# Performance work log

Measured on AMD Instinct MI355X. Metric: run time of the kernel, lower is better.

The kernel has to match this reference:

```python
import jax, jax.numpy as jnp
import numpy as np

M, T, D, H = 2, 2048, 1024, 16
HD = D // H
SCALE = 1.0 / np.sqrt(D).astype(np.float32)  # original divides by sqrt(emb_dim)


def setup_inputs() -> dict:
    key = jax.random.key(0)
    ks = jax.random.split(key, 8)
    def lin(k):
        kw, kb = jax.random.split(k)
        W = jax.random.normal(kw, (D, D), dtype=jnp.float32) * (1.0 / np.sqrt(D))
        b = jax.random.normal(kb, (D,), dtype=jnp.float32) * 0.01
        return W, b
    Wq, bq = lin(ks[0]); Wk, bk = lin(ks[1]); Wv, bv = lin(ks[2]); Wo, bo = lin(ks[3])
    Q = jax.random.normal(ks[4], (M, T, D), dtype=jnp.float32)
    K = jax.random.normal(ks[5], (M, T, D), dtype=jnp.float32)
    V = jax.random.normal(ks[6], (M, T, D), dtype=jnp.float32)
    mask = jnp.ones((M, 1, 1, T), dtype=jnp.int32)
    return {"Q": Q, "K": K, "V": V, "mask": mask,
            "Wq": Wq, "bq": bq, "Wk": Wk, "bk": bk,
            "Wv": Wv, "bv": bv, "Wo": Wo, "bo": bo}


def reference(Q, K, V, mask, Wq, bq, Wk, bk, Wv, bv, Wo, bo):
    m = Q.shape[0]
    # torch nn.Linear: y = x @ W.T + b
    q = (Q @ Wq.T + bq).reshape(m, -1, H, HD)  # (m, Tq, h, hd)
    k = (K @ Wk.T + bk).reshape(m, -1, H, HD)
    v = (V @ Wv.T + bv).reshape(m, -1, H, HD)
    energy = jnp.einsum('mqhd,mkhd->mhqk', q, k) * SCALE
    if mask is not None:
        energy = jnp.where(mask == 0, jnp.float32(-1e20), energy)
    attn = jax.nn.softmax(energy, axis=3)  # dropout is identity at inference
    out = jnp.einsum('mhqk,mkhd->mqhd', attn, v)  # (m, Tq, h, hd)
    concat = out.reshape(m, -1, H * HD)
    return concat @ Wo.T + bo
```

## Files before the change

kernel.cpp:

```cpp
#include <hip/hip_runtime.h>
#include <cstdint>
#include <cstddef>

#define T_SEQ 2048
#define D_EMB 1024
#define H_HEADS 16
#define MROWS 4096
#define SC2 (0.03125f * 1.44269504f)
#define MASKNEG (-1e30f)

typedef __attribute__((ext_vector_type(8))) short bf16x8;
typedef __attribute__((ext_vector_type(4))) float f32x4;
typedef __attribute__((ext_vector_type(16))) float f32x16;
typedef __attribute__((ext_vector_type(4))) unsigned short us4;

__device__ __forceinline__ unsigned short f2bf(float f) {
  union { float f; uint32_t u; } v; v.f = f;
  uint32_t u = v.u;
  return (unsigned short)((u + 0x7FFFu + ((u >> 16) & 1u)) >> 16);
}

__device__ __forceinline__ uint32_t cvtpk(float lo, float hi) {
  uint32_t r;
  asm("v_cvt_pk_bf16_f32 %0, %1, %2" : "=v"(r) : "v"(lo), "v"(hi));
  return r;
}

__device__ __forceinline__ float fexp2(float x) {
  float r;
  asm("v_exp_f32 %0, %1" : "=v"(r) : "v"(x));
  return r;
}

__device__ __forceinline__ void gl16(const void* g, void* l) {
  __builtin_amdgcn_global_load_lds(
      (const __attribute__((address_space(1))) unsigned int*)g,
      (__attribute__((address_space(3))) unsigned int*)l, 16, 0, 0);
}

__global__ __launch_bounds__(256) void cvt_all(
    const float* __restrict__ Q, const float* __restrict__ K, const float* __restrict__ V,
    const float* __restrict__ Wq, const float* __restrict__ Wk,
    const float* __restrict__ Wv, const float* __restrict__ Wo,
    unsigned short* __restrict__ Qb, unsigned short* __restrict__ Kb,
    unsigned short* __restrict__ Vb,
    unsigned short* __restrict__ Wqb, unsigned short* __restrict__ Wkb,
    unsigned short* __restrict__ Wvb, unsigned short* __restrict__ Wob) {
  int i = blockIdx.x * 256 + threadIdx.x;
  const float* src;
  unsigned short* dst;
  int j;
  if (i < 3145728) {
    int s = i >> 20;
    j = i & 1048575;
    src = (s == 0) ? Q : (s == 1) ? K : V;
    dst = (s == 0) ? Qb : (s == 1) ? Kb : Vb;
  } else {
    int k = i - 3145728;
    int s = k >> 18;
    j = k & 262143;
    src = (s == 0) ? Wq : (s == 1) ? Wk : (s == 2) ? Wv : Wo;
    dst = (s == 0) ? Wqb : (s == 1) ? Wkb : (s == 2) ? Wvb : Wob;
  }
  float4 f = ((const float4*)src)[j];
  us4 o;
  o[0] = f2bf(f.x); o[1] = f2bf(f.y); o[2] = f2bf(f.z); o[3] = f2bf(f.w);
  ((us4*)dst)[j] = o;
}

__global__ __launch_bounds__(256) void qkv_gemm(
    const unsigned short* __restrict__ Qb, const unsigned short* __restrict__ Kb,
    const unsigned short* __restrict__ Vb,
    const unsigned short* __restrict__ Wqb, const unsigned short* __restrict__ Wkb,
    const unsigned short* __restrict__ Wvb,
    const float* __restrict__ bq, const float* __restrict__ bk, const float* __restrict__ bv,
    unsigned short* __restrict__ qo, unsigned short* __restrict__ ko,
    unsigned short* __restrict__ vto) {
  const int swz = (blockIdx.x & 7) * 96 + (blockIdx.x >> 3);
  const int bx = swz & 7, by = (swz >> 3) & 31, z = swz >> 8;
  const unsigned short* A = (z == 0) ? Qb : (z == 1) ? Kb : Vb;
  const unsigned short* W = (z == 0) ? Wqb : (z == 1) ? Wkb : Wvb;
  const float* bias = (z == 0) ? bq : (z == 1) ? bk : bv;

  __shared__ __align__(16) unsigned short Asm[2][128 * 32];
  __shared__ __align__(16) unsigned short Bsm[2][128 * 32];

  const int tid = threadIdx.x;
  const int lane = tid & 63, w = tid >> 6;
  const int fq = lane >> 4, fr = lane & 15;
  const int brow = by * 128, bcol = bx * 128;
  const int wr = (w >> 1) * 64, wc = (w & 1) * 64;

  f32x4 acc[4][4] = {};

#define QKV_STAGE(buf, k0)                                                     \
  {                                                                            \
    _Pragma("unroll") for (int it = 0; it < 2; ++it) {                         \
      int idx = it * 256 + tid;                                                \
      int row = idx >> 2, ce = (idx & 3) * 8;                                  \
      gl16(&A[(size_t)(brow + row) * D_EMB + (k0) + ce],                       \
           (char*)Asm[buf] + idx * 16);                                        \
      gl16(&W[(size_t)(bcol + row) * D_EMB + (k0) + ce],                       \
           (char*)Bsm[buf] + idx * 16);                                        \
    }                                                                          \
  }

#define QKV_COMPUTE(buf)                                                       \
  {                                                                            \
    bf16x8 af[4], bfr[4];                                                      \
    _Pragma("unroll") for (int i = 0; i < 4; ++i)                              \
        af[i] = *(const bf16x8*)((const char*)Asm[buf] +                       \
                                 (wr + i * 16 + fr) * 64 + fq * 16);           \
    _Pragma("unroll") for (int j = 0; j < 4; ++j)                              \
        bfr[j] = *(const bf16x8*)((const char*)Bsm[buf] +                      \
                                  (wc + j * 16 + fr) * 64 + fq * 16);          \
    _Pragma("unroll") for (int i = 0; i < 4; ++i)                              \
        _Pragma("unroll") for (int j = 0; j < 4; ++j)                          \
            acc[i][j] = __builtin_amdgcn_mfma_f32_16x16x32_bf16(               \
                af[i], bfr[j], acc[i][j], 0, 0, 0);                            \
  }

  QKV_STAGE(0, 0);
  __syncthreads();
#pragma unroll 1
  for (int t = 0; t < 32; t += 2) {
    QKV_STAGE(1, (t + 1) * 32);
    QKV_COMPUTE(0);
    __syncthreads();
    if (t + 2 < 32) QKV_STAGE(0, (t + 2) * 32);
    QKV_COMPUTE(1);
    __syncthreads();
  }

#pragma unroll
  for (int i = 0; i < 4; ++i) {
#pragma unroll
    for (int j = 0; j < 4; ++j) {
      int r0 = brow + wr + i * 16 + fq * 4;
      int cc = bcol + wc + j * 16 + fr;
      float bb = bias[cc];
      if (z < 2) {
        unsigned short* O = (z == 0) ? qo : ko;
        float sc = (z == 0) ? SC2 : 1.0f;
#pragma unroll
        for (int q = 0; q < 4; ++q)
          O[(size_t)(r0 + q) * D_EMB + cc] = f2bf((acc[i][j][q] + bb) * sc);
      } else {
        int hh = cc >> 6, dd = cc & 63;
        int mm = r0 >> 11, tt = r0 & 2047;
        us4 pk;
#pragma unroll
        for (int q = 0; q < 4; ++q) pk[q] = f2bf(acc[i][j][q] + bb);
        *(us4*)&vto[((size_t)((mm * H_HEADS + hh) * 64 + dd)) * T_SEQ + tt] = pk;
      }
    }
  }
}

__global__ __launch_bounds__(256) void out_gemm(const unsigned short* __restrict__ Ab,
                                                const unsigned short* __restrict__ Wb,
                                                const float* __restrict__ bias,
                                                float* __restrict__ Out) {
  const int swz = (blockIdx.x & 7) * 64 + (blockIdx.x >> 3);
  const int bx = swz & 15, by = swz >> 4;

  __shared__ __align__(16) unsigned short Asm[2][128 * 32];
  __shared__ __align__(16) unsigned short Bsm[2][64 * 32];
  const int tid = threadIdx.x;
  const int lane = tid & 63, w = tid >> 6;
  const int fq = lane >> 4, fr = lane & 15;
  const int brow = by * 128, bcol = bx * 64;
  const int wr = w * 32;

  f32x4 acc[2][4] = {};

#define OUT_STAGE(buf, k0)                                                     \
  {                                                                            \
    _Pragma("unroll") for (int it = 0; it < 2; ++it) {                         \
      int idx = it * 256 + tid;                                                \
      int row = idx >> 2, ce = (idx & 3) * 8;                                  \
      gl16(&Ab[(size_t)(brow + row) * D_EMB + (k0) + ce],                      \
           (char*)Asm[buf] + idx * 16);                                        \
    }                                                                          \
    {                                                                          \
      int row = tid >> 2, ce = (tid & 3) * 8;                                  \
      gl16(&Wb[(size_t)(bcol + row) * D_EMB + (k0) + ce],                      \
           (char*)Bsm[buf] + tid * 16);                                        \
    }                                                                          \
  }

#define OUT_COMPUTE(buf)                                                       \
  {                                                                            \
    bf16x8 af[2], bfr[4];                                                      \
    _Pragma("unroll") for (int i = 0; i < 2; ++i)                              \
        af[i] = *(const bf16x8*)((const char*)Asm[buf] +                       \
                                 (wr + i * 16 + fr) * 64 + fq * 16);           \
    _Pragma("unroll") for (int j = 0; j < 4; ++j)                              \
        bfr[j] = *(const bf16x8*)((const char*)Bsm[buf] +                      \
                                  (j * 16 + fr) * 64 + fq * 16);               \
    _Pragma("unroll") for (int i = 0; i < 2; ++i)                              \
        _Pragma("unroll") for (int j = 0; j < 4; ++j)                          \
            acc[i][j] = __builtin_amdgcn_mfma_f32_16x16x32_bf16(               \
                af[i], bfr[j], acc[i][j], 0, 0, 0);                            \
  }

  OUT_STAGE(0, 0);
  __syncthreads();
#pragma unroll 1
  for (int t = 0; t < 32; t += 2) {
    OUT_STAGE(1, (t + 1) * 32);
    OUT_COMPUTE(0);
    __syncthreads();
    if (t + 2 < 32) OUT_STAGE(0, (t + 2) * 32);
    OUT_COMPUTE(1);
    __syncthreads();
  }

#pragma unroll
  for (int i = 0; i < 2; ++i)
#pragma unroll
    for (int j = 0; j < 4; ++j) {
      int r0 = brow + wr + i * 16 + fq * 4;
      int cc = bcol + j * 16 + fr;
      float bb = bias[cc];
#pragma unroll
      for (int q = 0; q < 4; ++q)
        Out[(size_t)(r0 + q) * D_EMB + cc] = acc[i][j][q] + bb;
    }
}

__global__ __launch_bounds__(256) void attn_fwd(const unsigned short* __restrict__ qb,
                                                const unsigned short* __restrict__ kb,
                                                const unsigned short* __restrict__ vtb,
                                                const int* __restrict__ maskg,
                                                unsigned short* __restrict__ outb) {
  const int swzb = (blockIdx.x & 7) * 64 + (blockIdx.x >> 3);
  const int qt = swzb & 15, h = (swzb >> 4) & 15, mI = swzb >> 8;
  const int tid = threadIdx.x;
  const int lane = tid & 63, w = tid >> 6;
  const int lq = lane & 31, h2 = lane >> 5;
  const int xk = (lq & 7) << 4;
  const int vx = (lq & 7) << 4;

  __shared__ __align__(16) unsigned short Ksm[128 * 64];
  __shared__ __align__(16) unsigned short Vsm[64 * 128];
  __shared__ __align__(16) char Pw[4][2304];
  __shared__ __align__(16) float Msm[128];
  __shared__ int moks[16];

  char* KsmB = (char*)Ksm;
  char* VsmB = (char*)Vsm;
  char* PwB = Pw[w];

  if (tid < 16) moks[tid] = 1;
  __syncthreads();
  {
    int bad = 0;
    const int4* mg = (const int4*)&maskg[mI * T_SEQ + tid * 8];
    int4 a = mg[0], b = mg[1];
    bad |= (a.x == 0) | (a.y == 0) | (a.z == 0) | (a.w == 0);
    bad |= (b.x == 0) | (b.y == 0) | (b.z == 0) | (b.w == 0);
    if (bad) moks[tid >> 4] = 0;
  }
  __syncthreads();
  int okbits = 0;
#pragma unroll
  for (int i = 0; i < 16; ++i) okbits |= (moks[i] != 0) << i;

  const int qrow = qt * 128 + w * 32 + lq;
  bf16x8 qf[4];
#pragma unroll
  for (int db = 0; db < 4; ++db)
    qf[db] = *(const bf16x8*)&qb[((size_t)(mI * T_SEQ) + qrow) * D_EMB + h * 64 + db * 16 + h2 * 8];

  f32x16 oacc[2] = {};
  f32x16 liv = {};

  const unsigned short* kpan = kb + (size_t)(mI * T_SEQ) * D_EMB + h * 64;
  const unsigned short* vpan = vtb + (size_t)(mI * H_HEADS + h) * 64 * T_SEQ;

#pragma unroll 1
  for (int k0 = 0; k0 < T_SEQ; k0 += 128) {
    const int ok = (okbits >> (k0 >> 7)) & 1;
#pragma unroll
    for (int it = 0; it < 4; ++it) {
      int idx = it * 256 + tid;
      int row = idx >> 3;
      int sb = ((idx & 7) * 16) ^ ((row & 7) << 4);
      gl16(kpan + (size_t)(k0 + row) * D_EMB + (sb >> 1), KsmB + idx * 16);
    }
#pragma unroll
    for (int it = 0; it < 4; ++it) {
      int idx = it * 256 + tid;
      int row = idx >> 4;
      int sb = ((idx & 15) * 16) ^ ((row & 7) << 4);
      gl16(vpan + (size_t)row * T_SEQ + k0 + (sb >> 1), VsmB + idx * 16);
    }
    if (!ok && tid < 128) Msm[tid] = (maskg[mI * T_SEQ + k0 + tid] == 0) ? MASKNEG : 0.f;
    __syncthreads();

#pragma unroll 1
    for (int kbk = 0; kbk < 4; ++kbk) {
      f32x16 sv = {};
      const char* kr = KsmB + (kbk * 32 + lq) * 128;
#pragma unroll
      for (int db = 0; db < 4; ++db) {
        bf16x8 kf = *(const bf16x8*)(kr + ((db * 32 + h2 * 16) ^ xk));
        sv = __builtin_amdgcn_mfma_f32_32x32x16_bf16(kf, qf[db], sv, 0, 0, 0);
      }
      if (!ok) {
#pragma unroll
        for (int rg = 0; rg < 4; ++rg) {
          f32x4 mk = *(const f32x4*)&Msm[kbk * 32 + rg * 8 + h2 * 4];
          sv[rg * 4 + 0] += mk[0]; sv[rg * 4 + 1] += mk[1];
          sv[rg * 4 + 2] += mk[2]; sv[rg * 4 + 3] += mk[3];
        }
      }
#pragma unroll
      for (int r = 0; r < 16; ++r) sv[r] = fexp2(sv[r]);
      liv += sv;
#pragma unroll
      for (int rg = 0; rg < 4; ++rg) {
        uint2 pw;
        pw.x = cvtpk(sv[rg * 4 + 0], sv[rg * 4 + 1]);
        pw.y = cvtpk(sv[rg * 4 + 2], sv[rg * 4 + 3]);
        *(uint2*)(PwB + lq * 72 + rg * 16 + h2 * 8) = pw;
      }
      bf16x8 pf[2];
#pragma unroll
      for (int s = 0; s < 2; ++s) {
        union { bf16x8 v; uint2 d[2]; } u;
        u.d[0] = *(const uint2*)(PwB + lq * 72 + s * 32 + h2 * 16);
        u.d[1] = *(const uint2*)(PwB + lq * 72 + s * 32 + h2 * 16 + 8);
        pf[s] = u.v;
      }
#pragma unroll
      for (int vb = 0; vb < 2; ++vb) {
        const char* vbase = VsmB + (vb * 32 + lq) * 256;
#pragma unroll
        for (int s = 0; s < 2; ++s) {
          bf16x8 vf = *(const bf16x8*)(vbase + ((kbk * 64 + s * 32 + h2 * 16) ^ vx));
          oacc[vb] = __builtin_amdgcn_mfma_f32_32x32x16_bf16(vf, pf[s], oacc[vb], 0, 0, 0);
        }
      }
    }
    __syncthreads();
  }

  float li = 0.f;
#pragma unroll
  for (int r = 0; r < 16; ++r) li += liv[r];
  li += __shfl_xor(li, 32);
  float inv = 1.f / li;
  size_t orow = (size_t)(mI * T_SEQ + qrow) * D_EMB + h * 64;
#pragma unroll
  for (int vb = 0; vb < 2; ++vb)
#pragma unroll
    for (int rg = 0; rg < 4; ++rg) {
      uint2 ow;
      ow.x = cvtpk(oacc[vb][rg * 4 + 0] * inv, oacc[vb][rg * 4 + 1] * inv);
      ow.y = cvtpk(oacc[vb][rg * 4 + 2] * inv, oacc[vb][rg * 4 + 3] * inv);
      *(uint2*)&outb[orow + vb * 32 + rg * 8 + h2 * 4] = ow;
    }
}

extern "C" void kernel_launch(void* const* d_in, const int* in_sizes, int n_in,
                              void* d_out, int out_size, void* d_ws, size_t ws_size,
                              hipStream_t stream) {
  const float* Q  = (const float*)d_in[0];
  const float* K  = (const float*)d_in[1];
  const float* V  = (const float*)d_in[2];
  const int* mask = (const int*)d_in[3];
  const float* Wq = (const float*)d_in[4];
  const float* bq = (const float*)d_in[5];
  const float* Wk = (const float*)d_in[6];
  const float* bk = (const float*)d_in[7];
  const float* Wv = (const float*)d_in[8];
  const float* bv = (const float*)d_in[9];
  const float* Wo = (const float*)d_in[10];
  const float* bo = (const float*)d_in[11];

  uint8_t* ws = (uint8_t*)d_ws;
  const size_t MB = 1u << 20;
  unsigned short* Wq_b = (unsigned short*)(ws + 0 * MB);
  unsigned short* Wk_b = (unsigned short*)(ws + 2 * MB);
  unsigned short* Wv_b = (unsigned short*)(ws + 4 * MB);
  unsigned short* Wo_b = (unsigned short*)(ws + 6 * MB);
  unsigned short* q_b  = (unsigned short*)(ws + 8 * MB);
  unsigned short* k_b  = (unsigned short*)(ws + 16 * MB);
  unsigned short* vt_b = (unsigned short*)(ws + 24 * MB);
  unsigned short* Qb   = (unsigned short*)(ws + 32 * MB);
  unsigned short* Kb   = (unsigned short*)(ws + 40 * MB);
  unsigned short* Vb   = (unsigned short*)(ws + 48 * MB);
  unsigned short* cc_b = (unsigned short*)(ws + 32 * MB);

  cvt_all<<<dim3(16384), dim3(256), 0, stream>>>(Q, K, V, Wq, Wk, Wv, Wo,
                                                 Qb, Kb, Vb, Wq_b, Wk_b, Wv_b, Wo_b);

  qkv_gemm<<<dim3(768), dim3(256), 0, stream>>>(
      Qb, Kb, Vb, Wq_b, Wk_b, Wv_b, bq, bk, bv, q_b, k_b, vt_b);

  attn_fwd<<<dim3(512), dim3(256), 0, stream>>>(
      q_b, k_b, vt_b, mask, cc_b);

  out_gemm<<<dim3(512), dim3(256), 0, stream>>>(
      cc_b, Wo_b, bo, (float*)d_out);
}
```

Before: 141.7 us.

## Split attention over key halves with a combine pass and shuffle-based P transpose

Attention now splits the key dimension in two, doubling the grid to 1024 blocks. Each block writes unnormalised bf16 partial outputs and partial row sums, and a new combine kernel adds the halves and normalises them. Separately, the P-matrix relayout through per-wave LDS is replaced by cross-half-wave shuffles and selects, which removes the LDS buffer and its stores and loads. The cost is an extra kernel launch, extra global traffic for the partials, and an extra bf16 rounding of the unnormalised partial sums.

```diff
diff --git a/kernel.cpp b/kernel.cpp
--- a/kernel.cpp
+++ b/kernel.cpp
@@ -30,6 +30,11 @@
   float r;
   asm("v_exp_f32 %0, %1" : "=v"(r) : "v"(x));
   return r;
+}
+
+__device__ __forceinline__ float bf2f(unsigned short u) {
+  union { uint32_t u; float f; } v; v.u = ((uint32_t)u) << 16;
+  return v.f;
 }
 
 __device__ __forceinline__ void gl16(const void* g, void* l) {
@@ -233,9 +238,10 @@
                                                 const unsigned short* __restrict__ kb,
                                                 const unsigned short* __restrict__ vtb,
                                                 const int* __restrict__ maskg,
-                                                unsigned short* __restrict__ outb) {
-  const int swzb = (blockIdx.x & 7) * 64 + (blockIdx.x >> 3);
-  const int qt = swzb & 15, h = (swzb >> 4) & 15, mI = swzb >> 8;
+                                                unsigned short* __restrict__ opart,
+                                                float* __restrict__ lipart) {
+  const int swzb = (blockIdx.x & 7) * 128 + (blockIdx.x >> 3);
+  const int qt = swzb & 15, h = (swzb >> 4) & 15, mI = (swzb >> 8) & 1, sp = swzb >> 9;
   const int tid = threadIdx.x;
   const int lane = tid & 63, w = tid >> 6;
   const int lq = lane & 31, h2 = lane >> 5;
@@ -244,13 +250,11 @@
 
   __shared__ __align__(16) unsigned short Ksm[128 * 64];
   __shared__ __align__(16) unsigned short Vsm[64 * 128];
-  __shared__ __align__(16) char Pw[4][2304];
   __shared__ __align__(16) float Msm[128];
   __shared__ int moks[16];
 
   char* KsmB = (char*)Ksm;
   char* VsmB = (char*)Vsm;
-  char* PwB = Pw[w];
 
   if (tid < 16) moks[tid] = 1;
   __syncthreads();
@@ -280,23 +284,25 @@
   const unsigned short* vpan = vtb + (size_t)(mI * H_HEADS + h) * 64 * T_SEQ;
 
 #pragma unroll 1
-  for (int k0 = 0; k0 < T_SEQ; k0 += 128) {
-    const int ok = (okbits >> (k0 >> 7)) & 1;
+  for (int t = sp * 8; t < sp * 8 + 8; ++t) {
+    const int okv = (okbits >> t) & 1;
+    const int k0s = t * 128;
 #pragma unroll
     for (int it = 0; it < 4; ++it) {
       int idx = it * 256 + tid;
       int row = idx >> 3;
       int sb = ((idx & 7) * 16) ^ ((row & 7) << 4);
-      gl16(kpan + (size_t)(k0 + row) * D_EMB + (sb >> 1), KsmB + idx * 16);
+      gl16(kpan + (size_t)(k0s + row) * D_EMB + (sb >> 1), KsmB + idx * 16);
     }
 #pragma unroll
     for (int it = 0; it < 4; ++it) {
       int idx = it * 256 + tid;
       int row = idx >> 4;
       int sb = ((idx & 15) * 16) ^ ((row & 7) << 4);
-      gl16(vpan + (size_t)row * T_SEQ + k0 + (sb >> 1), VsmB + idx * 16);
-    }
-    if (!ok && tid < 128) Msm[tid] = (maskg[mI * T_SEQ + k0 + tid] == 0) ? MASKNEG : 0.f;
+      gl16(vpan + (size_t)row * T_SEQ + k0s + (sb >> 1), VsmB + idx * 16);
+    }
+    if (!okv && tid < 128)
+      Msm[tid] = (maskg[mI * T_SEQ + k0s + tid] == 0) ? MASKNEG : 0.f;
     __syncthreads();
 
 #pragma unroll 1
@@ -308,7 +314,7 @@
         bf16x8 kf = *(const bf16x8*)(kr + ((db * 32 + h2 * 16) ^ xk));
         sv = __builtin_amdgcn_mfma_f32_32x32x16_bf16(kf, qf[db], sv, 0, 0, 0);
       }
-      if (!ok) {
+      if (!okv) {
 #pragma unroll
         for (int rg = 0; rg < 4; ++rg) {
           f32x4 mk = *(const f32x4*)&Msm[kbk * 32 + rg * 8 + h2 * 4];
@@ -319,20 +325,26 @@
 #pragma unroll
       for (int r = 0; r < 16; ++r) sv[r] = fexp2(sv[r]);
       liv += sv;
-#pragma unroll
-      for (int rg = 0; rg < 4; ++rg) {
-        uint2 pw;
-        pw.x = cvtpk(sv[rg * 4 + 0], sv[rg * 4 + 1]);
-        pw.y = cvtpk(sv[rg * 4 + 2], sv[rg * 4 + 3]);
-        *(uint2*)(PwB + lq * 72 + rg * 16 + h2 * 8) = pw;
-      }
+      uint32_t w0 = cvtpk(sv[0], sv[1]), w1 = cvtpk(sv[2], sv[3]);
+      uint32_t w2 = cvtpk(sv[4], sv[5]), w3 = cvtpk(sv[6], sv[7]);
+      uint32_t w4 = cvtpk(sv[8], sv[9]), w5 = cvtpk(sv[10], sv[11]);
+      uint32_t w6 = cvtpk(sv[12], sv[13]), w7 = cvtpk(sv[14], sv[15]);
+      uint32_t x0 = __shfl_xor(w0, 32), x1 = __shfl_xor(w1, 32);
+      uint32_t x2 = __shfl_xor(w2, 32), x3 = __shfl_xor(w3, 32);
+      uint32_t x4 = __shfl_xor(w4, 32), x5 = __shfl_xor(w5, 32);
+      uint32_t x6 = __shfl_xor(w6, 32), x7 = __shfl_xor(w7, 32);
       bf16x8 pf[2];
-#pragma unroll
-      for (int s = 0; s < 2; ++s) {
-        union { bf16x8 v; uint2 d[2]; } u;
-        u.d[0] = *(const uint2*)(PwB + lq * 72 + s * 32 + h2 * 16);
-        u.d[1] = *(const uint2*)(PwB + lq * 72 + s * 32 + h2 * 16 + 8);
-        pf[s] = u.v;
+      {
+        union { bf16x8 v; uint32_t u[4]; } u_;
+        u_.u[0] = h2 ? x2 : w0; u_.u[1] = h2 ? x3 : w1;
+        u_.u[2] = h2 ? w2 : x0; u_.u[3] = h2 ? w3 : x1;
+        pf[0] = u_.v;
+      }
+      {
+        union { bf16x8 v; uint32_t u[4]; } u_;
+        u_.u[0] = h2 ? x6 : w4; u_.u[1] = h2 ? x7 : w5;
+        u_.u[2] = h2 ? w6 : x4; u_.u[3] = h2 ? w7 : x5;
+        pf[1] = u_.v;
       }
 #pragma unroll
       for (int vb = 0; vb < 2; ++vb) {
@@ -351,17 +363,44 @@
 #pragma unroll
   for (int r = 0; r < 16; ++r) li += liv[r];
   li += __shfl_xor(li, 32);
-  float inv = 1.f / li;
+
+  unsigned short* op = opart + (size_t)sp * ((size_t)MROWS * D_EMB);
   size_t orow = (size_t)(mI * T_SEQ + qrow) * D_EMB + h * 64;
 #pragma unroll
   for (int vb = 0; vb < 2; ++vb)
 #pragma unroll
     for (int rg = 0; rg < 4; ++rg) {
       uint2 ow;
-      ow.x = cvtpk(oacc[vb][rg * 4 + 0] * inv, oacc[vb][rg * 4 + 1] * inv);
-      ow.y = cvtpk(oacc[vb][rg * 4 + 2] * inv, oacc[vb][rg * 4 + 3] * inv);
-      *(uint2*)&outb[orow + vb * 32 + rg * 8 + h2 * 4] = ow;
-    }
+      ow.x = cvtpk(oacc[vb][rg * 4 + 0], oacc[vb][rg * 4 + 1]);
+      ow.y = cvtpk(oacc[vb][rg * 4 + 2], oacc[vb][rg * 4 + 3]);
+      *(uint2*)&op[orow + vb * 32 + rg * 8 + h2 * 4] = ow;
+    }
+  if (h2 == 0)
+    lipart[((size_t)sp * MROWS + mI * T_SEQ + qrow) * H_HEADS + h] = li;
+}
+
+__global__ __launch_bounds__(256) void combine(const unsigned short* __restrict__ opart,
+                                               const float* __restrict__ lipart,
+                                               unsigned short* __restrict__ cc) {
+  int i = blockIdx.x * 256 + threadIdx.x;
+  int row = i >> 7;
+  int c8 = i & 127;
+  int h = c8 >> 3;
+  float l0 = lipart[(size_t)row * H_HEADS + h];
+  float l1 = lipart[((size_t)MROWS + row) * H_HEADS + h];
+  float inv = 1.f / (l0 + l1);
+  size_t off = (size_t)row * D_EMB + c8 * 8;
+  us4 a0 = *(const us4*)&opart[off];
+  us4 a1 = *(const us4*)&opart[off + 4];
+  us4 b0 = *(const us4*)&opart[(size_t)MROWS * D_EMB + off];
+  us4 b1 = *(const us4*)&opart[(size_t)MROWS * D_EMB + off + 4];
+  uint2 o0, o1;
+  o0.x = cvtpk((bf2f(a0[0]) + bf2f(b0[0])) * inv, (bf2f(a0[1]) + bf2f(b0[1])) * inv);
+  o0.y = cvtpk((bf2f(a0[2]) + bf2f(b0[2])) * inv, (bf2f(a0[3]) + bf2f(b0[3])) * inv);
+  o1.x = cvtpk((bf2f(a1[0]) + bf2f(b1[0])) * inv, (bf2f(a1[1]) + bf2f(b1[1])) * inv);
+  o1.y = cvtpk((bf2f(a1[2]) + bf2f(b1[2])) * inv, (bf2f(a1[3]) + bf2f(b1[3])) * inv);
+  *(uint2*)&cc[off] = o0;
+  *(uint2*)&cc[off + 4] = o1;
 }
 
 extern "C" void kernel_launch(void* const* d_in, const int* in_sizes, int n_in,
@@ -389,10 +428,12 @@
   unsigned short* q_b  = (unsigned short*)(ws + 8 * MB);
   unsigned short* k_b  = (unsigned short*)(ws + 16 * MB);
   unsigned short* vt_b = (unsigned short*)(ws + 24 * MB);
-  unsigned short* Qb   = (unsigned short*)(ws + 32 * MB);
-  unsigned short* Kb   = (unsigned short*)(ws + 40 * MB);
-  unsigned short* Vb   = (unsigned short*)(ws + 48 * MB);
-  unsigned short* cc_b = (unsigned short*)(ws + 32 * MB);
+  unsigned short* Qb    = (unsigned short*)(ws + 32 * MB);
+  unsigned short* Kb    = (unsigned short*)(ws + 40 * MB);
+  unsigned short* Vb    = (unsigned short*)(ws + 48 * MB);
+  unsigned short* opart = (unsigned short*)(ws + 32 * MB);
+  unsigned short* cc_b  = (unsigned short*)(ws + 48 * MB);
+  float*          lipart = (float*)(ws + 56 * MB);
 
   cvt_all<<<dim3(16384), dim3(256), 0, stream>>>(Q, K, V, Wq, Wk, Wv, Wo,
                                                  Qb, Kb, Vb, Wq_b, Wk_b, Wv_b, Wo_b);
@@ -400,8 +441,10 @@
   qkv_gemm<<<dim3(768), dim3(256), 0, stream>>>(
       Qb, Kb, Vb, Wq_b, Wk_b, Wv_b, bq, bk, bv, q_b, k_b, vt_b);
 
-  attn_fwd<<<dim3(512), dim3(256), 0, stream>>>(
-      q_b, k_b, vt_b, mask, cc_b);
+  attn_fwd<<<dim3(1024), dim3(256), 0, stream>>>(
+      q_b, k_b, vt_b, mask, opart, lipart);
+
+  combine<<<dim3(2048), dim3(256), 0, stream>>>(opart, lipart, cc_b);
 
   out_gemm<<<dim3(512), dim3(256), 0, stream>>>(
       cc_b, Wo_b, bo, (float*)d_out);
```

New measurement: 151.0 us. +6.6%, slower.
